# Performance work log

Hardware: AMD Instinct MI355X
Metric: run time of the kernel (lower is better)

Reference implementation:

```python
import jax, jax.numpy as jnp
import numpy as np
from jax import lax

N, CIN, COUT, H, W = 16, 512, 256, 32, 32
EPS = 1e-5


def _conv(x, w, b, pad_h, pad_w):
    # x: [N,Cin,H,W], w: [Cout,Cin,kh,kw], pad = ((top,bottom),(left,right))
    y = lax.conv_general_dilated(
        x, w, window_strides=(1, 1), padding=(pad_h, pad_w),
        dimension_numbers=("NCHW", "OIHW", "NCHW"))
    return y + b[None, :, None, None]


def setup_inputs() -> dict:
    key = jax.random.key(0)
    ks = jax.random.split(key, 12)
    s = 0.02
    return {
        "x": jax.random.normal(ks[0], (N, CIN, H, W), jnp.float32),
        "w1": jax.random.normal(ks[1], (COUT, CIN, 3, 3), jnp.float32) * s,
        "b1": jax.random.normal(ks[2], (COUT,), jnp.float32) * s,
        "w2": jax.random.normal(ks[3], (COUT, CIN, 2, 3), jnp.float32) * s,
        "b2": jax.random.normal(ks[4], (COUT,), jnp.float32) * s,
        "w3": jax.random.normal(ks[5], (COUT, CIN, 3, 2), jnp.float32) * s,
        "b3": jax.random.normal(ks[6], (COUT,), jnp.float32) * s,
        "w4": jax.random.normal(ks[7], (COUT, CIN, 2, 2), jnp.float32) * s,
        "b4": jax.random.normal(ks[8], (COUT,), jnp.float32) * s,
        "gamma": jnp.ones((COUT,), jnp.float32),
        "beta": jnp.zeros((COUT,), jnp.float32),
    }


def reference(x, w1, b1, w2, b2, w3, b3, w4, b4, gamma, beta):
    # torch F.pad(l,r,t,b) -> lax padding ((top,bottom),(left,right))
    o1 = _conv(x, w1, b1, (1, 1), (1, 1))  # 3x3, pad (1,1,1,1) -> [N,Cout,H,W]
    o2 = _conv(x, w2, b2, (1, 0), (1, 1))  # 2x3, pad (1,1,1,0)
    o3 = _conv(x, w3, b3, (1, 1), (1, 0))  # 3x2, pad (1,0,1,1)
    o4 = _conv(x, w4, b4, (1, 0), (1, 0))  # 2x2, pad (1,0,1,0)
    # pixel-shuffle interleave: o1->(even,even), o2->(odd,even), o3->(even,odd), o4->(odd,odd)
    row_even = jnp.stack([o1, o3], axis=-1).reshape(N, COUT, H, 2 * W)
    row_odd = jnp.stack([o2, o4], axis=-1).reshape(N, COUT, H, 2 * W)
    y = jnp.stack([row_even, row_odd], axis=-2).reshape(N, COUT, 2 * H, 2 * W)
    # BatchNorm2d, training mode: biased batch stats over (N,H,W)
    mean = jnp.mean(y, axis=(0, 2, 3), keepdims=True)
    var = jnp.mean(jnp.square(y - mean), axis=(0, 2, 3), keepdims=True)
    normed = (y - mean) * lax.rsqrt(var + EPS)
    normed = normed * gamma[None, :, None, None] + beta[None, :, None, None]
    return jax.nn.relu(normed)
```

## Files before the change

kernel.cpp:

```cpp
#include <hip/hip_runtime.h>
#include <hip/hip_bf16.h>


typedef unsigned short ushort_t;
typedef __attribute__((ext_vector_type(8))) short short8;
typedef __attribute__((ext_vector_type(4))) float floatx4;
typedef __attribute__((ext_vector_type(2))) float floatx2;
typedef __attribute__((ext_vector_type(4))) unsigned short u16x4;
typedef __attribute__((ext_vector_type(8))) unsigned short u16x8;
typedef __attribute__((ext_vector_type(4))) unsigned int u32x4;

#define XT_OFF    0u
#define WT_OFF    18939904u
#define BIAS_OFF  28377088u
#define STATS_OFF 28381184u

#define NSITES 204

#define ASYNC16(g, l) __builtin_amdgcn_global_load_lds( \
    (const __attribute__((address_space(1))) void*)(g), \
    (__attribute__((address_space(3))) void*)(l), 16, 0, 0)

__device__ __forceinline__ ushort_t f2bf(float f) {
  unsigned int u = __builtin_bit_cast(unsigned int, f);
  u += 0x7fffu + ((u >> 16) & 1u);
  return (ushort_t)(u >> 16);
}

__global__ __launch_bounds__(256) void prep_x(const float* __restrict__ x,
                                              ushort_t* __restrict__ xt) {
  const int b = blockIdx.x;
  const int n = b / 34, hp = b % 34;
  const int t = threadIdx.x;
  ushort_t* dst = xt + (size_t)(n * 34 + hp) * (34 * 512);
  if (hp == 0 || hp == 33) {
    u32x4 z = {0u, 0u, 0u, 0u};
    for (int i = t; i < 2176; i += 256) ((u32x4*)dst)[i] = z;
    return;
  }
  const int h = hp - 1;
  {
    u32x4 z = {0u, 0u, 0u, 0u};
    if (t < 64) ((u32x4*)dst)[t] = z;
    else if (t < 128) ((u32x4*)(dst + 33 * 512))[t - 64] = z;
  }
  __shared__ ushort_t lds[128 * 36];
  const size_t base = (size_t)n * 524288 + (size_t)h * 32;
  for (int ci0 = 0; ci0 < 512; ci0 += 128) {
    __syncthreads();
    {
      const int cil = t >> 3;
      const int w4 = (t & 7) << 2;
#pragma unroll
      for (int cc = 0; cc < 4; ++cc) {
        const int ci = cil + cc * 32;
        floatx4 v = *(const floatx4*)(x + base + (size_t)(ci0 + ci) * 1024 + w4);
        u16x4 hv;
#pragma unroll
        for (int j = 0; j < 4; ++j) hv[j] = f2bf(v[j]);
        *(u16x4*)&lds[ci * 36 + w4] = hv;
      }
    }
    __syncthreads();
    {
      const int w = t & 31;
      const int j8 = t >> 5;
#pragma unroll
      for (int cc2 = 0; cc2 < 2; ++cc2) {
        const int cil = cc2 * 64 + j8 * 8;
        u16x8 v;
#pragma unroll
        for (int j = 0; j < 8; ++j) v[j] = lds[(cil + j) * 36 + w];
        *(u16x8*)(dst + (w + 1) * 512 + ci0 + cil) = v;
      }
    }
  }
}

__global__ __launch_bounds__(256) void prep_w(
    const float* __restrict__ w1, const float* __restrict__ w2,
    const float* __restrict__ w3, const float* __restrict__ w4,
    const float* __restrict__ b1, const float* __restrict__ b2,
    const float* __restrict__ b3, const float* __restrict__ b4,
    ushort_t* __restrict__ wt, float* __restrict__ bias) {
  const int nout = blockIdx.x;
  const int q = nout >> 8, co = nout & 255;
  const int row = co * 4 + q;
  const int t = threadIdx.x;
  const float* wsrc; const float* bsrc; int khl, kwl;
  if (q == 0)      { wsrc = w1; bsrc = b1; khl = 3; kwl = 3; }
  else if (q == 1) { wsrc = w2; bsrc = b2; khl = 2; kwl = 3; }
  else if (q == 2) { wsrc = w3; bsrc = b3; khl = 3; kwl = 2; }
  else             { wsrc = w4; bsrc = b4; khl = 2; kwl = 2; }
  if (t == 0) bias[row] = bsrc[co];
  ushort_t* dst = wt + (size_t)row * 4608;
  for (int tap = 0; tap < 9; ++tap) {
    const int dh = tap / 3, dw = tap % 3;
    const bool valid = (dh < khl) && (dw < kwl);
#pragma unroll
    for (int cc = 0; cc < 2; ++cc) {
      const int ci = cc * 256 + t;
      ushort_t v = 0;
      if (valid) v = f2bf(wsrc[(((size_t)co * 512 + ci) * khl + dh) * kwl + dw]);
      dst[tap * 512 + ci] = v;
    }
  }
}

__global__ void zero_stats(float* __restrict__ stats) {
  stats[threadIdx.x] = 0.f;
}

__global__ __launch_bounds__(256) void gemm_kernel(
    const ushort_t* __restrict__ xt, const ushort_t* __restrict__ wt,
    const float* __restrict__ bias, float* __restrict__ out,
    float* __restrict__ stats) {
  __shared__ char ldsX[NSITES * 128];
  __shared__ char ldsW[2][128 * 128];
  const int tid = threadIdx.x;
  const int bx = blockIdx.x;
  const int bn = bx & 7, bm = bx >> 3;
  const int n0 = bn << 7;
  const int n_img = bm >> 3;
  const int h0p = (bm & 7) << 2;
  const int wv = tid >> 6, lane = tid & 63;
  const int ri = lane & 15, kg = lane >> 4;
  const int wm = (wv & 1) << 6, wn = (wv >> 1) << 6;

  const char* xgp[7];
  char* xlp[7];
  {
    const char* xg = (const char*)(xt + (size_t)(n_img * 34 + h0p) * (34 * 512));
#pragma unroll
    for (int p = 0; p < 7; ++p) {
      const int idx = p * 256 + tid;
      const int site = idx >> 3, slot = idx & 7;
      const int c = slot ^ (site & 7);
      xgp[p] = xg + site * 1024 + (c << 4);
      xlp[p] = ldsX + idx * 16;
    }
  }
  const char* wgp[4];
  char* wlp0[4];
  char* wlp1[4];
#pragma unroll
  for (int p = 0; p < 4; ++p) {
    const int idx = p * 256 + tid;
    const int row = idx >> 3, slot = idx & 7;
    const int c = slot ^ (row & 7);
    wgp[p] = (const char*)wt + (size_t)(n0 + row) * 9216 + (c << 4);
    wlp0[p] = ldsW[0] + idx * 16;
    wlp1[p] = ldsW[1] + idx * 16;
  }

  floatx4 acc[4][4] = {};

  int arow[4], bsite[4];
#pragma unroll
  for (int f = 0; f < 4; ++f) arow[f] = wn + (f << 4) + ri;
#pragma unroll
  for (int fj = 0; fj < 4; ++fj)
    bsite[fj] = ((wm >> 5) + (fj >> 1)) * 34 + ((fj & 1) << 4) + ri;

  for (int chunk = 0; chunk < 8; ++chunk) {
    const int cb = chunk << 7;
#pragma unroll
    for (int p = 0; p < 6; ++p) ASYNC16(xgp[p] + cb, xlp[p]);
    if (tid < 96) ASYNC16(xgp[6] + cb, xlp[6]);
#pragma unroll
    for (int p = 0; p < 4; ++p) ASYNC16(wgp[p] + cb, wlp0[p]);
    __syncthreads();
#pragma unroll
    for (int tap = 0; tap < 9; ++tap) {
      if (tap < 8) {
        const int noff = ((tap + 1) << 10) + cb;
        if (tap & 1) {
#pragma unroll
          for (int p = 0; p < 4; ++p) ASYNC16(wgp[p] + noff, wlp0[p]);
        } else {
#pragma unroll
          for (int p = 0; p < 4; ++p) ASYNC16(wgp[p] + noff, wlp1[p]);
        }
      }
      const char* wb = ldsW[tap & 1];
      const int tapo = ((tap / 3) * 34 + (tap % 3)) * 128;
#pragma unroll
      for (int ks = 0; ks < 2; ++ks) {
        const int c = (ks << 2) + kg;
        short8 a4[4], b4[4];
#pragma unroll
        for (int f = 0; f < 4; ++f)
          a4[f] = *(const short8*)(wb + arow[f] * 128 +
                                   ((c ^ (arow[f] & 7)) << 4));
#pragma unroll
        for (int fj = 0; fj < 4; ++fj) {
          const int sadr = bsite[fj] * 128 + tapo;
          const int srow = bsite[fj] + (tap / 3) * 34 + (tap % 3);
          b4[fj] = *(const short8*)(ldsX + sadr + ((c ^ (srow & 7)) << 4));
        }
#pragma unroll
        for (int fi = 0; fi < 4; ++fi)
#pragma unroll
          for (int fj = 0; fj < 4; ++fj)
            acc[fi][fj] = __builtin_amdgcn_mfma_f32_16x16x32_bf16(
                a4[fi], b4[fj], acc[fi][fj], 0, 0, 0);
      }
      __syncthreads();
    }
  }

  const int quad = kg, colL = ri;
#pragma unroll
  for (int fi = 0; fi < 4; ++fi) {
    const int co = ((n0 + wn + (fi << 4)) >> 2) + quad;
    const floatx4 bv = *(const floatx4*)(bias + n0 + wn + (fi << 4) + (quad << 2));
    float s = 0.f, s2 = 0.f;
    float* obase = out + ((size_t)(n_img * 256 + co) << 12);
#pragma unroll
    for (int fj = 0; fj < 4; ++fj) {
      const int mb = wm + (fj << 4) + colL;
      const int hl = mb >> 5, w = mb & 31;
      const int h = h0p + hl;
      float v0 = acc[fi][fj][0] + bv[0];
      float v1 = acc[fi][fj][1] + bv[1];
      float v2 = acc[fi][fj][2] + bv[2];
      float v3 = acc[fi][fj][3] + bv[3];
      s += (v0 + v1) + (v2 + v3);
      s2 += v0 * v0 + v1 * v1 + v2 * v2 + v3 * v3;
      float* p = obase + (h << 7) + (w << 1);
      floatx2 e = {v0, v2};
      floatx2 o = {v1, v3};
      *(floatx2*)p = e;
      *(floatx2*)(p + 64) = o;
    }
#pragma unroll
    for (int off = 1; off < 16; off <<= 1) {
      s += __shfl_xor(s, off);
      s2 += __shfl_xor(s2, off);
    }
    if (colL == 0) {
      atomicAdd(&stats[co], s);
      atomicAdd(&stats[256 + co], s2);
    }
  }
}

__global__ __launch_bounds__(256) void bn_apply(
    float* __restrict__ y, const float* __restrict__ stats,
    const float* __restrict__ gamma, const float* __restrict__ beta) {
  const int b = blockIdx.x;
  const int co = b & 255;
  const int t = threadIdx.x;
  const float mean = stats[co] * (1.f / 65536.f);
  const float var = stats[256 + co] * (1.f / 65536.f) - mean * mean;
  const float rstd = rsqrtf(var + 1e-5f);
  const float scale = rstd * gamma[co];
  const float shift = beta[co] - mean * scale;
  float* p = y + (size_t)b * 4096;
#pragma unroll
  for (int it = 0; it < 4; ++it) {
    floatx4* q = (floatx4*)(p + (it * 256 + t) * 4);
    floatx4 v = *q;
#pragma unroll
    for (int e = 0; e < 4; ++e) v[e] = fmaxf(v[e] * scale + shift, 0.f);
    *q = v;
  }
}

extern "C" void kernel_launch(void* const* d_in, const int* in_sizes, int n_in,
                              void* d_out, int out_size, void* d_ws,
                              size_t ws_size, hipStream_t stream) {
  const float* x  = (const float*)d_in[0];
  const float* w1 = (const float*)d_in[1];
  const float* b1 = (const float*)d_in[2];
  const float* w2 = (const float*)d_in[3];
  const float* b2 = (const float*)d_in[4];
  const float* w3 = (const float*)d_in[5];
  const float* b3 = (const float*)d_in[6];
  const float* w4 = (const float*)d_in[7];
  const float* b4 = (const float*)d_in[8];
  const float* gamma = (const float*)d_in[9];
  const float* beta  = (const float*)d_in[10];
  float* out = (float*)d_out;

  char* ws = (char*)d_ws;
  ushort_t* xt   = (ushort_t*)(ws + XT_OFF);
  ushort_t* wt   = (ushort_t*)(ws + WT_OFF);
  float*    bias = (float*)(ws + BIAS_OFF);
  float*    st   = (float*)(ws + STATS_OFF);

  zero_stats<<<1, 512, 0, stream>>>(st);
  prep_x<<<16 * 34, 256, 0, stream>>>(x, xt);
  prep_w<<<1024, 256, 0, stream>>>(w1, w2, w3, w4, b1, b2, b3, b4, wt, bias);
  gemm_kernel<<<1024, 256, 0, stream>>>(xt, wt, bias, out, st);
  bn_apply<<<4096, 256, 0, stream>>>(out, st, gamma, beta);
}
```

Measured before the change: 272.6 us.

## Group weight rows by conv branch and skip zero-padded taps per block

Weight rows are now laid out branch-major, so each GEMM block handles a single conv branch (3x3, 2x3, 3x2 or 2x2). Each block then loops only over that branch's valid taps, taken from a packed tap list, instead of all 9 padded taps. This removes the MFMA work and weight loads spent on the zero padding. In exchange the tap loop now has a runtime trip count (no full unroll), blocks are unevenly loaded, and the epilogue writes strided scalar stores with four times as many stat atomics.

```diff
diff --git a/kernel.cpp b/kernel.cpp
--- a/kernel.cpp
+++ b/kernel.cpp
@@ -85,7 +85,7 @@
     ushort_t* __restrict__ wt, float* __restrict__ bias) {
   const int nout = blockIdx.x;
   const int q = nout >> 8, co = nout & 255;
-  const int row = co * 4 + q;
+  const int row = nout;
   const int t = threadIdx.x;
   const float* wsrc; const float* bsrc; int khl, kwl;
   if (q == 0)      { wsrc = w1; bsrc = b1; khl = 3; kwl = 3; }
@@ -120,12 +120,19 @@
   const int tid = threadIdx.x;
   const int bx = blockIdx.x;
   const int bn = bx & 7, bm = bx >> 3;
+  const int q = bn >> 1;
   const int n0 = bn << 7;
   const int n_img = bm >> 3;
   const int h0p = (bm & 7) << 2;
   const int wv = tid >> 6, lane = tid & 63;
   const int ri = lane & 15, kg = lane >> 4;
   const int wm = (wv & 1) << 6, wn = (wv >> 1) << 6;
+
+  const int ntaps = (q == 0) ? 9 : ((q == 3) ? 4 : 6);
+  const unsigned long long tl =
+      (q == 0) ? 0x876543210ull :
+      (q == 1) ? 0x543210ull :
+      (q == 2) ? 0x764310ull : 0x4310ull;
 
   const char* xgp[7];
   char* xlp[7];
@@ -170,11 +177,12 @@
 #pragma unroll
     for (int p = 0; p < 4; ++p) ASYNC16(wgp[p] + cb, wlp0[p]);
     __syncthreads();
-#pragma unroll
-    for (int tap = 0; tap < 9; ++tap) {
-      if (tap < 8) {
-        const int noff = ((tap + 1) << 10) + cb;
-        if (tap & 1) {
+    for (int ti = 0; ti < ntaps; ++ti) {
+      const int tap = (int)((tl >> (ti << 2)) & 15ull);
+      if (ti + 1 < ntaps) {
+        const int ntap = (int)((tl >> ((ti + 1) << 2)) & 15ull);
+        const int noff = (ntap << 10) + cb;
+        if (ti & 1) {
 #pragma unroll
           for (int p = 0; p < 4; ++p) ASYNC16(wgp[p] + noff, wlp0[p]);
         } else {
@@ -182,8 +190,8 @@
           for (int p = 0; p < 4; ++p) ASYNC16(wgp[p] + noff, wlp1[p]);
         }
       }
-      const char* wb = ldsW[tap & 1];
-      const int tapo = ((tap / 3) * 34 + (tap % 3)) * 128;
+      const char* wb = ldsW[ti & 1];
+      const int tsite = (tap / 3) * 34 + (tap % 3);
 #pragma unroll
       for (int ks = 0; ks < 2; ++ks) {
         const int c = (ks << 2) + kg;
@@ -194,9 +202,8 @@
                                    ((c ^ (arow[f] & 7)) << 4));
 #pragma unroll
         for (int fj = 0; fj < 4; ++fj) {
-          const int sadr = bsite[fj] * 128 + tapo;
-          const int srow = bsite[fj] + (tap / 3) * 34 + (tap % 3);
-          b4[fj] = *(const short8*)(ldsX + sadr + ((c ^ (srow & 7)) << 4));
+          const int srow = bsite[fj] + tsite;
+          b4[fj] = *(const short8*)(ldsX + srow * 128 + ((c ^ (srow & 7)) << 4));
         }
 #pragma unroll
         for (int fi = 0; fi < 4; ++fi)
@@ -210,37 +217,43 @@
   }
 
   const int quad = kg, colL = ri;
+  const int dh = q & 1;
+  const int dw = q >> 1;
+  const int pos_off = (dh << 6) + dw;
 #pragma unroll
   for (int fi = 0; fi < 4; ++fi) {
-    const int co = ((n0 + wn + (fi << 4)) >> 2) + quad;
-    const floatx4 bv = *(const floatx4*)(bias + n0 + wn + (fi << 4) + (quad << 2));
-    float s = 0.f, s2 = 0.f;
-    float* obase = out + ((size_t)(n_img * 256 + co) << 12);
+    const int cobase = ((bn & 1) << 7) + wn + (fi << 4) + (quad << 2);
+    const floatx4 bv = *(const floatx4*)(bias + (q << 8) + cobase);
+    floatx4 sj = {};
+    floatx4 s2j = {};
+    float* ob = out + (((size_t)(n_img * 256 + cobase)) << 12) + pos_off;
 #pragma unroll
     for (int fj = 0; fj < 4; ++fj) {
       const int mb = wm + (fj << 4) + colL;
-      const int hl = mb >> 5, w = mb & 31;
-      const int h = h0p + hl;
-      float v0 = acc[fi][fj][0] + bv[0];
-      float v1 = acc[fi][fj][1] + bv[1];
-      float v2 = acc[fi][fj][2] + bv[2];
-      float v3 = acc[fi][fj][3] + bv[3];
-      s += (v0 + v1) + (v2 + v3);
-      s2 += v0 * v0 + v1 * v1 + v2 * v2 + v3 * v3;
-      float* p = obase + (h << 7) + (w << 1);
-      floatx2 e = {v0, v2};
-      floatx2 o = {v1, v3};
-      *(floatx2*)p = e;
-      *(floatx2*)(p + 64) = o;
+      const int h = h0p + (mb >> 5), w = mb & 31;
+      const int off = (h << 7) + (w << 1);
+#pragma unroll
+      for (int j = 0; j < 4; ++j) {
+        const float v = acc[fi][fj][j] + bv[j];
+        sj[j] += v;
+        s2j[j] += v * v;
+        ob[((size_t)j << 12) + off] = v;
+      }
     }
 #pragma unroll
     for (int off = 1; off < 16; off <<= 1) {
-      s += __shfl_xor(s, off);
-      s2 += __shfl_xor(s2, off);
+#pragma unroll
+      for (int j = 0; j < 4; ++j) {
+        sj[j] += __shfl_xor(sj[j], off);
+        s2j[j] += __shfl_xor(s2j[j], off);
+      }
     }
     if (colL == 0) {
-      atomicAdd(&stats[co], s);
-      atomicAdd(&stats[256 + co], s2);
+#pragma unroll
+      for (int j = 0; j < 4; ++j) {
+        atomicAdd(&stats[cobase + j], sj[j]);
+        atomicAdd(&stats[256 + cobase + j], s2j[j]);
+      }
     }
   }
 }
```

Result: slower. 334.5 us (+22.7%).

## Reorder weight rows by kernel height so 2-row convs skip zero taps

Applied to the files above, without the earlier changes.

The fused weight matrix's output rows are re-laid out so the 3-row-tall kernels (3x3, 3x2) fill the first half of the N dimension and the 2-row-tall kernels (2x3, 2x2) fill the second half. GEMM blocks in the second half then loop over 6 taps instead of 9, skipping the bottom tap row, which is all zero padding for those kernels. This removes MFMA work and weight loads that only multiply zeros. The epilogue is rewritten to match the new row mapping: each quad now holds two channels, so it keeps two sets of BN statistics and issues twice as many atomics. The tap loop bound now depends on the block, so the loop is no longer fully unrolled, and blocks now do unequal amounts of work.

```diff
diff --git a/kernel.cpp b/kernel.cpp
--- a/kernel.cpp
+++ b/kernel.cpp
@@ -85,7 +85,7 @@
     ushort_t* __restrict__ wt, float* __restrict__ bias) {
   const int nout = blockIdx.x;
   const int q = nout >> 8, co = nout & 255;
-  const int row = co * 4 + q;
+  const int row = ((q & 1) << 9) + (co << 1) + (q >> 1);
   const int t = threadIdx.x;
   const float* wsrc; const float* bsrc; int khl, kwl;
   if (q == 0)      { wsrc = w1; bsrc = b1; khl = 3; kwl = 3; }
@@ -127,6 +127,8 @@
   const int ri = lane & 15, kg = lane >> 4;
   const int wm = (wv & 1) << 6, wn = (wv >> 1) << 6;
 
+  const int ntaps = (bn < 4) ? 9 : 6;
+
   const char* xgp[7];
   char* xlp[7];
   {
@@ -170,9 +172,8 @@
 #pragma unroll
     for (int p = 0; p < 4; ++p) ASYNC16(wgp[p] + cb, wlp0[p]);
     __syncthreads();
-#pragma unroll
-    for (int tap = 0; tap < 9; ++tap) {
-      if (tap < 8) {
+    for (int tap = 0; tap < ntaps; ++tap) {
+      if (tap + 1 < ntaps) {
         const int noff = ((tap + 1) << 10) + cb;
         if (tap & 1) {
 #pragma unroll
@@ -183,7 +184,7 @@
         }
       }
       const char* wb = ldsW[tap & 1];
-      const int tapo = ((tap / 3) * 34 + (tap % 3)) * 128;
+      const int tsite = (tap / 3) * 34 + (tap % 3);
 #pragma unroll
       for (int ks = 0; ks < 2; ++ks) {
         const int c = (ks << 2) + kg;
@@ -194,9 +195,8 @@
                                    ((c ^ (arow[f] & 7)) << 4));
 #pragma unroll
         for (int fj = 0; fj < 4; ++fj) {
-          const int sadr = bsite[fj] * 128 + tapo;
-          const int srow = bsite[fj] + (tap / 3) * 34 + (tap % 3);
-          b4[fj] = *(const short8*)(ldsX + sadr + ((c ^ (srow & 7)) << 4));
+          const int srow = bsite[fj] + tsite;
+          b4[fj] = *(const short8*)(ldsX + srow * 128 + ((c ^ (srow & 7)) << 4));
         }
 #pragma unroll
         for (int fi = 0; fi < 4; ++fi)
@@ -210,37 +210,44 @@
   }
 
   const int quad = kg, colL = ri;
+  const int dh6 = (bn >> 2) << 6;
 #pragma unroll
   for (int fi = 0; fi < 4; ++fi) {
-    const int co = ((n0 + wn + (fi << 4)) >> 2) + quad;
-    const floatx4 bv = *(const floatx4*)(bias + n0 + wn + (fi << 4) + (quad << 2));
-    float s = 0.f, s2 = 0.f;
-    float* obase = out + ((size_t)(n_img * 256 + co) << 12);
+    const int rbase = n0 + wn + (fi << 4) + (quad << 2);
+    const floatx4 bv = *(const floatx4*)(bias + rbase);
+    const int co = (rbase & 511) >> 1;
+    float sA = 0.f, s2A = 0.f, sB = 0.f, s2B = 0.f;
+    float* ob = out + (((size_t)(n_img * 256 + co)) << 12) + dh6;
 #pragma unroll
     for (int fj = 0; fj < 4; ++fj) {
       const int mb = wm + (fj << 4) + colL;
-      const int hl = mb >> 5, w = mb & 31;
-      const int h = h0p + hl;
-      float v0 = acc[fi][fj][0] + bv[0];
-      float v1 = acc[fi][fj][1] + bv[1];
-      float v2 = acc[fi][fj][2] + bv[2];
-      float v3 = acc[fi][fj][3] + bv[3];
-      s += (v0 + v1) + (v2 + v3);
-      s2 += v0 * v0 + v1 * v1 + v2 * v2 + v3 * v3;
-      float* p = obase + (h << 7) + (w << 1);
-      floatx2 e = {v0, v2};
-      floatx2 o = {v1, v3};
-      *(floatx2*)p = e;
-      *(floatx2*)(p + 64) = o;
+      const int h = h0p + (mb >> 5), w = mb & 31;
+      const float v0 = acc[fi][fj][0] + bv[0];
+      const float v1 = acc[fi][fj][1] + bv[1];
+      const float v2 = acc[fi][fj][2] + bv[2];
+      const float v3 = acc[fi][fj][3] + bv[3];
+      sA += v0 + v1;
+      s2A += v0 * v0 + v1 * v1;
+      sB += v2 + v3;
+      s2B += v2 * v2 + v3 * v3;
+      float* p = ob + (h << 7) + (w << 1);
+      floatx2 eA = {v0, v1};
+      floatx2 eB = {v2, v3};
+      *(floatx2*)p = eA;
+      *(floatx2*)(p + 4096) = eB;
     }
 #pragma unroll
     for (int off = 1; off < 16; off <<= 1) {
-      s += __shfl_xor(s, off);
-      s2 += __shfl_xor(s2, off);
+      sA += __shfl_xor(sA, off);
+      s2A += __shfl_xor(s2A, off);
+      sB += __shfl_xor(sB, off);
+      s2B += __shfl_xor(s2B, off);
     }
     if (colL == 0) {
-      atomicAdd(&stats[co], s);
-      atomicAdd(&stats[256 + co], s2);
+      atomicAdd(&stats[co], sA);
+      atomicAdd(&stats[256 + co], s2A);
+      atomicAdd(&stats[co + 1], sB);
+      atomicAdd(&stats[256 + co + 1], s2B);
     }
   }
 }
```

Result: slower. 312.2 us (+14.6%).
